# Kernel tuning notes

Hardware: AMD Instinct MI355X
Metric: run time of the kernel (lower is better)

Reference implementation:

```python
import jax, jax.numpy as jnp
import numpy as np

DIM = 256
N_EMBED = 1024
COMMITMENT_COST = 0.25


def setup_inputs() -> dict:
    key = jax.random.key(0)
    k1, k2 = jax.random.split(key)
    z = jax.random.normal(k1, (16, DIM, 64, 64), dtype=jnp.float32)
    lim = 1.0 / (2 * N_EMBED)
    embed_w = jax.random.uniform(k2, (N_EMBED, DIM), dtype=jnp.float32,
                                 minval=-lim, maxval=lim)
    return {"z": z, "embed_w": embed_w}


def reference(z, embed_w):
    # z: [B, C, H, W] -> [B, H, W, C]
    zp = jnp.transpose(z, (0, 2, 3, 1))
    B, H, W, C = zp.shape
    zf = zp.reshape(-1, C)  # [N, dim]
    # Squared euclidean distances to each codebook entry: [N, n_embed]
    d = (jnp.sum(zf * zf, axis=1, keepdims=True)
         + jnp.sum(embed_w * embed_w, axis=1)
         - 2.0 * jnp.matmul(zf, embed_w.T))
    idx = jnp.argmin(d, axis=1)  # [N]
    # Codebook lookup (equivalent to one-hot @ embed_w)
    z_q = embed_w[idx].reshape(zp.shape)  # [B, H, W, C]
    # VQ loss: codebook + commitment terms
    sg = jax.lax.stop_gradient
    loss = (jnp.mean((sg(z_q) - zp) ** 2)
            + COMMITMENT_COST * jnp.mean((z_q - sg(zp)) ** 2))
    # Straight-through estimator
    z_q_st = zp + sg(z_q - zp)
    # Perplexity from code usage histogram
    n = zf.shape[0]
    counts = jax.ops.segment_sum(jnp.ones((n,), jnp.float32), idx,
                                 num_segments=N_EMBED)
    e_mean = counts / n
    perplexity = jnp.exp(-jnp.sum(e_mean * jnp.log(e_mean + 1e-10)))
    z_q_out = jnp.transpose(z_q_st, (0, 3, 1, 2))  # back to [B, C, H, W]
    return loss, z_q_out, idx[:, None], perplexity
```

## Files before the change

kernel.cpp:

```cpp
#include <hip/hip_runtime.h>

#define BATCH 16
#define CDIM  256
#define HDIM  64
#define WDIM  64
#define NQ    65536
#define NE    1024
#define BM    32
#define KB    16

#define ZQ_OFF   1
#define IDX_OFF  16777217
#define PERP_OFF 16842753

#define WS_EE_OFF    0
#define WS_HIST_OFF  4096
#define WS_LOSS_OFF  8192
#define WS_WT_OFF    16384

__device__ __forceinline__ float pw128_sq(const float* __restrict__ p) {
    float r[8];
#pragma unroll
    for (int j = 0; j < 8; j++) r[j] = __fmul_rn(p[j], p[j]);
#pragma unroll
    for (int i = 8; i < 128; i += 8) {
#pragma unroll
        for (int j = 0; j < 8; j++) r[j] = __fadd_rn(r[j], __fmul_rn(p[i + j], p[i + j]));
    }
    return __fadd_rn(__fadd_rn(__fadd_rn(r[0], r[1]), __fadd_rn(r[2], r[3])),
                     __fadd_rn(__fadd_rn(r[4], r[5]), __fadd_rn(r[6], r[7])));
}

__global__ void vq_prep(const float* __restrict__ W, float* __restrict__ ee,
                        int* __restrict__ hist, double* __restrict__ loss_part) {
    int t = blockIdx.x * 256 + threadIdx.x;
    hist[t] = 0;
    if (t < 256) loss_part[t] = 0.0;
    const float* p = W + (size_t)t * CDIM;
    ee[t] = __fadd_rn(pw128_sq(p), pw128_sq(p + 128));
}

__global__ void vq_transpose(const float* __restrict__ W, float* __restrict__ WT) {
    __shared__ float T[64][65];
    const int e0 = (blockIdx.x & 15) * 64;
    const int k0 = (blockIdx.x >> 4) * 64;
    const int r  = threadIdx.x >> 4;
    const int c4 = threadIdx.x & 15;
#pragma unroll
    for (int s = 0; s < 4; s++) {
        float4 v = *(const float4*)(W + (size_t)(e0 + s * 16 + r) * CDIM + k0 + c4 * 4);
        T[s * 16 + r][c4 * 4 + 0] = v.x;
        T[s * 16 + r][c4 * 4 + 1] = v.y;
        T[s * 16 + r][c4 * 4 + 2] = v.z;
        T[s * 16 + r][c4 * 4 + 3] = v.w;
    }
    __syncthreads();
#pragma unroll
    for (int s = 0; s < 4; s++) {
        float4 o;
        o.x = T[c4 * 4 + 0][s * 16 + r];
        o.y = T[c4 * 4 + 1][s * 16 + r];
        o.z = T[c4 * 4 + 2][s * 16 + r];
        o.w = T[c4 * 4 + 3][s * 16 + r];
        *(float4*)(WT + (size_t)(k0 + s * 16 + r) * NE + e0 + c4 * 4) = o;
    }
}

__global__ __launch_bounds__(256, 4)
void vq_argmin(const float* __restrict__ z, const float* __restrict__ WT,
               const float* __restrict__ ee, float* __restrict__ out_idx,
               int* __restrict__ hist) {
    __shared__ __align__(16) float S[8192];
    __shared__ float zz_s[BM];
    __shared__ float tmp2[64];
    __shared__ float pD[BM][8];
    __shared__ int   pI[BM][8];

    float (*A)[BM]       = (float (*)[BM])S;
    float (*Bs)[KB][256] = (float (*)[KB][256])S;
    float (*redD)[64]    = (float (*)[64])S;
    int   (*redI)[64]    = (int (*)[64])(S + 2048);

    const int t    = threadIdx.x;
    const int lane = t & 63;
    const int wv   = t >> 6;
    const int n0   = blockIdx.x * BM;
    const int b    = n0 >> 12;
    const int h    = (n0 >> 6) & 63;
    const int w0   = n0 & 63;

    const float* zb = z + (size_t)b * (CDIM * HDIM * WDIM) + (size_t)h * WDIM + w0;
#pragma unroll
    for (int v = 0; v < 8; v++) {
        int idx4 = v * 256 + t;
        int c  = idx4 >> 3;
        int w4 = idx4 & 7;
        *(float4*)(&A[c][w4 * 4]) = *(const float4*)(zb + (size_t)c * (HDIM * WDIM) + w4 * 4);
    }
    __syncthreads();

    if (t < 64) {
        int q = t >> 1, base = (t & 1) * 128;
        float r[8];
#pragma unroll
        for (int j = 0; j < 8; j++) { float x = A[base + j][q]; r[j] = __fmul_rn(x, x); }
        for (int i = 8; i < 128; i += 8) {
#pragma unroll
            for (int j = 0; j < 8; j++) { float x = A[base + i + j][q]; r[j] = __fadd_rn(r[j], __fmul_rn(x, x)); }
        }
        tmp2[t] = __fadd_rn(__fadd_rn(__fadd_rn(r[0], r[1]), __fadd_rn(r[2], r[3])),
                            __fadd_rn(__fadd_rn(r[4], r[5]), __fadd_rn(r[6], r[7])));
    }
    __syncthreads();
    if (t < BM) zz_s[t] = __fadd_rn(tmp2[2 * t], tmp2[2 * t + 1]);

    const int tx  = t & 63;
    const int q0  = wv * 8;
    const int q0u = __builtin_amdgcn_readfirstlane(q0);
    const float* aG = zb + q0u;

    auto stage = [&](int sec, int skc, int nb) {
#pragma unroll
        for (int v = 0; v < 4; v++) {
            const int r_ = v * 4 + wv;
            const float* g_ = WT + (size_t)(skc * KB + r_) * NE + sec * 256 + lane * 4;
            __builtin_amdgcn_global_load_lds(
                (const __attribute__((address_space(1))) void*)g_,
                (__attribute__((address_space(3))) void*)(&Bs[nb][r_][0]),
                16, 0, 0);
        }
    };

    float bestD[8]; int bestI[8];
#pragma unroll
    for (int i = 0; i < 8; i++) { bestD[i] = 3.0e38f; bestI[i] = 0; }

    stage(0, 0, 0);
    __syncthreads();

    for (int ec = 0; ec < 4; ec++) {
        float acc[8][4];
#pragma unroll
        for (int i = 0; i < 8; i++)
#pragma unroll
            for (int j = 0; j < 4; j++) acc[i][j] = 0.0f;

        for (int kc = 0; kc < 16; kc++) {
            const int cur = kc & 1;
            {
                int nkc = kc + 1, nec = ec;
                if (nkc == 16) { nkc = 0; nec++; }
                if (nec < 4) stage(nec, nkc, cur ^ 1);
            }
            const int kb = kc * KB;
#pragma unroll 4
            for (int k2 = 0; k2 < KB; k2++) {
                const float4 b4 = *(const float4*)(&Bs[cur][k2][tx * 4]);
                const float* ar = aG + (size_t)(kb + k2) * (HDIM * WDIM);
                float av[8];
#pragma unroll
                for (int i = 0; i < 8; i++) av[i] = ar[i];
                float bv[4] = {b4.x, b4.y, b4.z, b4.w};
#pragma unroll
                for (int i = 0; i < 8; i++)
#pragma unroll
                    for (int j = 0; j < 4; j++)
                        acc[i][j] = __fmaf_rn(av[i], bv[j], acc[i][j]);
            }
            __syncthreads();
        }

        const int e0 = ec * 256 + tx * 4;
        float4 ee4 = *(const float4*)(ee + e0);
        float eev[4] = {ee4.x, ee4.y, ee4.z, ee4.w};
#pragma unroll
        for (int i = 0; i < 8; i++) {
            float zzq = zz_s[q0 + i];
#pragma unroll
            for (int j = 0; j < 4; j++) {
                float s = __fadd_rn(zzq, eev[j]);
                float d = __fsub_rn(s, __fadd_rn(acc[i][j], acc[i][j]));
                if (d < bestD[i]) { bestD[i] = d; bestI[i] = e0 + j; }
            }
        }
    }

    __syncthreads();
#pragma unroll
    for (int i = 0; i < 8; i++) { redD[q0 + i][tx] = bestD[i]; redI[q0 + i][tx] = bestI[i]; }
    __syncthreads();
    {
        int q = t >> 3, s = t & 7;
        float bd = redD[q][s * 8]; int bi = redI[q][s * 8];
#pragma unroll
        for (int u = 1; u < 8; u++) {
            float d2 = redD[q][s * 8 + u]; int i2 = redI[q][s * 8 + u];
            if (d2 < bd || (d2 == bd && i2 < bi)) { bd = d2; bi = i2; }
        }
        pD[q][s] = bd; pI[q][s] = bi;
    }
    __syncthreads();
    if (t < BM) {
        float bd = pD[t][0]; int bi = pI[t][0];
#pragma unroll
        for (int u = 1; u < 8; u++) {
            float d2 = pD[t][u]; int i2 = pI[t][u];
            if (d2 < bd || (d2 == bd && i2 < bi)) { bd = d2; bi = i2; }
        }
        out_idx[n0 + t] = (float)bi;
        atomicAdd(&hist[bi], 1);
    }
}

__global__ void vq_gather(const float* __restrict__ z, const float* __restrict__ W,
                          const float* __restrict__ idxf, float* __restrict__ zq_out,
                          double* __restrict__ loss_part) {
    const int gid = blockIdx.x * 256 + threadIdx.x;
    const int w4 = gid & 15;
    const int r  = gid >> 4;
    const int h  = r & 63;
    const int c  = (r >> 6) & 255;
    const int b  = r >> 14;
    const size_t off = (((size_t)(b * CDIM + c) * HDIM + h) * WDIM) + w4 * 4;
    const float4 zp = *(const float4*)(z + off);
    const int n = b * 4096 + h * 64 + w4 * 4;

    float zpv[4] = {zp.x, zp.y, zp.z, zp.w};
    float ov[4];
    double ls = 0.0;
#pragma unroll
    for (int l = 0; l < 4; l++) {
        int idx = (int)idxf[n + l];
        float zq = W[(size_t)idx * CDIM + c];
        float t1 = __fsub_rn(zq, zpv[l]);
        ov[l] = __fadd_rn(zpv[l], t1);
        ls += (double)t1 * (double)t1;
    }
    float4 o = {ov[0], ov[1], ov[2], ov[3]};
    *(float4*)(zq_out + off) = o;

#pragma unroll
    for (int s = 32; s > 0; s >>= 1) ls += __shfl_down(ls, s, 64);
    __shared__ double wsum[4];
    if ((threadIdx.x & 63) == 0) wsum[threadIdx.x >> 6] = ls;
    __syncthreads();
    if (threadIdx.x == 0) {
        double v = wsum[0] + wsum[1] + wsum[2] + wsum[3];
        atomicAdd(&loss_part[blockIdx.x & 255], v);
    }
}

__global__ void vq_final(const double* __restrict__ loss_part, const int* __restrict__ hist,
                         float* __restrict__ d_out) {
    __shared__ double s1[256], s2[256];
    const int t = threadIdx.x;
    double v = loss_part[t];
    double pv = 0.0;
#pragma unroll
    for (int j = 0; j < 4; j++) {
        int cnt = hist[t * 4 + j];
        double em = (double)cnt / 65536.0;
        pv += em * log(em + 1e-10);
    }
    s1[t] = v; s2[t] = pv;
    __syncthreads();
    for (int st = 128; st > 0; st >>= 1) {
        if (t < st) { s1[t] += s1[t + st]; s2[t] += s2[t + st]; }
        __syncthreads();
    }
    if (t == 0) {
        float m = (float)(s1[0] / 16777216.0);
        d_out[0] = 1.25f * m;
        d_out[PERP_OFF] = (float)exp(-s2[0]);
    }
}

extern "C" void kernel_launch(void* const* d_in, const int* in_sizes, int n_in,
                              void* d_out, int out_size, void* d_ws, size_t ws_size,
                              hipStream_t stream) {
    const float* z = (const float*)d_in[0];
    const float* W = (const float*)d_in[1];
    float* out = (float*)d_out;

    float*  ee        = (float*)((char*)d_ws + WS_EE_OFF);
    int*    hist      = (int*)((char*)d_ws + WS_HIST_OFF);
    double* loss_part = (double*)((char*)d_ws + WS_LOSS_OFF);
    float*  WT        = (float*)((char*)d_ws + WS_WT_OFF);

    vq_prep<<<4, 256, 0, stream>>>(W, ee, hist, loss_part);
    vq_transpose<<<64, 256, 0, stream>>>(W, WT);
    vq_argmin<<<NQ / BM, 256, 0, stream>>>(z, WT, ee, out + IDX_OFF, hist);
    vq_gather<<<(NQ * CDIM / 4) / 256, 256, 0, stream>>>(z, W, out + IDX_OFF, out + ZQ_OFF, loss_part);
    vq_final<<<1, 256, 0, stream>>>(loss_part, hist, out);
}
```

Measured before the change: 556.5 us.

## Software-pipeline z loads as float4 registers and halve B tile depth

Halves the codebook k-tile depth so each LDS buffer holds 8 rows, and adds register double-buffering of the z operand: float4 loads for the next 4 k-steps are issued before computing the current 4. Running best distance/index is kept in LDS reduction arrays (moved past the B buffers) instead of registers, which frees registers for the prefetch buffers. The stage loop now always prefetches, wrapping to section 0 at the end, so it does one redundant tile load. The intent is to hide global-load latency on z and cut register pressure, at the cost of twice as many block barriers per section.

```diff
diff --git a/kernel.cpp b/kernel.cpp
--- a/kernel.cpp
+++ b/kernel.cpp
@@ -7,7 +7,7 @@
 #define NQ    65536
 #define NE    1024
 #define BM    32
-#define KB    16
+#define KB    8
 
 #define ZQ_OFF   1
 #define IDX_OFF  16777217
@@ -78,8 +78,8 @@
 
     float (*A)[BM]       = (float (*)[BM])S;
     float (*Bs)[KB][256] = (float (*)[KB][256])S;
-    float (*redD)[64]    = (float (*)[64])S;
-    int   (*redI)[64]    = (int (*)[64])(S + 2048);
+    float (*redD)[64]    = (float (*)[64])(S + 4096);
+    int   (*redI)[64]    = (int   (*)[64])(S + 6144);
 
     const int t    = threadIdx.x;
     const int lane = t & 63;
@@ -114,16 +114,15 @@
     __syncthreads();
     if (t < BM) zz_s[t] = __fadd_rn(tmp2[2 * t], tmp2[2 * t + 1]);
 
-    const int tx  = t & 63;
-    const int q0  = wv * 8;
-    const int q0u = __builtin_amdgcn_readfirstlane(q0);
-    const float* aG = zb + q0u;
-
-    auto stage = [&](int sec, int skc, int nb) {
-#pragma unroll
-        for (int v = 0; v < 4; v++) {
+    const int tx = t & 63;
+    const int q0 = wv * 8;
+    const float* aq = zb + q0;
+
+    auto stage = [&](int ssec, int skc, int nb) {
+#pragma unroll
+        for (int v = 0; v < 2; v++) {
             const int r_ = v * 4 + wv;
-            const float* g_ = WT + (size_t)(skc * KB + r_) * NE + sec * 256 + lane * 4;
+            const float* g_ = WT + (size_t)(skc * KB + r_) * NE + ssec * 256 + lane * 4;
             __builtin_amdgcn_global_load_lds(
                 (const __attribute__((address_space(1))) void*)g_,
                 (__attribute__((address_space(3))) void*)(&Bs[nb][r_][0]),
@@ -131,73 +130,95 @@
         }
     };
 
-    float bestD[8]; int bestI[8];
-#pragma unroll
-    for (int i = 0; i < 8; i++) { bestD[i] = 3.0e38f; bestI[i] = 0; }
+    float4 av0[8], av1[8];
 
     stage(0, 0, 0);
-    __syncthreads();
-
-    for (int ec = 0; ec < 4; ec++) {
+#pragma unroll
+    for (int kk = 0; kk < 4; kk++) {
+        const float* ap = aq + (size_t)kk * 4096;
+        av0[kk * 2]     = *(const float4*)ap;
+        av0[kk * 2 + 1] = *(const float4*)(ap + 4);
+    }
+    __syncthreads();
+
+#define COMPUTE4(CUR, G, AV)                                                   \
+    {                                                                          \
+        _Pragma("unroll")                                                      \
+        for (int k2 = 0; k2 < 4; k2++) {                                       \
+            const float4 b4 = *(const float4*)(&Bs[CUR][(G) + k2][tx * 4]);    \
+            const float4 aL = AV[k2 * 2], aH = AV[k2 * 2 + 1];                 \
+            float avv[8] = {aL.x, aL.y, aL.z, aL.w, aH.x, aH.y, aH.z, aH.w};   \
+            float bvv[4] = {b4.x, b4.y, b4.z, b4.w};                           \
+            _Pragma("unroll")                                                  \
+            for (int i = 0; i < 8; i++)                                        \
+                _Pragma("unroll")                                              \
+                for (int j = 0; j < 4; j++)                                    \
+                    acc[i][j] = __fmaf_rn(avv[i], bvv[j], acc[i][j]);          \
+        }                                                                      \
+    }
+
+    for (int sec = 0; sec < 4; sec++) {
         float acc[8][4];
 #pragma unroll
         for (int i = 0; i < 8; i++)
 #pragma unroll
             for (int j = 0; j < 4; j++) acc[i][j] = 0.0f;
 
-        for (int kc = 0; kc < 16; kc++) {
+        for (int kc = 0; kc < 32; kc++) {
             const int cur = kc & 1;
             {
-                int nkc = kc + 1, nec = ec;
-                if (nkc == 16) { nkc = 0; nec++; }
-                if (nec < 4) stage(nec, nkc, cur ^ 1);
+                int nkc = kc + 1, nsec = sec;
+                if (nkc == 32) { nkc = 0; nsec = (sec + 1) & 3; }
+                stage(nsec, nkc, cur ^ 1);
             }
-            const int kb = kc * KB;
-#pragma unroll 4
-            for (int k2 = 0; k2 < KB; k2++) {
-                const float4 b4 = *(const float4*)(&Bs[cur][k2][tx * 4]);
-                const float* ar = aG + (size_t)(kb + k2) * (HDIM * WDIM);
-                float av[8];
-#pragma unroll
-                for (int i = 0; i < 8; i++) av[i] = ar[i];
-                float bv[4] = {b4.x, b4.y, b4.z, b4.w};
-#pragma unroll
-                for (int i = 0; i < 8; i++)
-#pragma unroll
-                    for (int j = 0; j < 4; j++)
-                        acc[i][j] = __fmaf_rn(av[i], bv[j], acc[i][j]);
+            const int kbase = kc * KB;
+#pragma unroll
+            for (int kk = 0; kk < 4; kk++) {
+                const float* ap = aq + (size_t)((kbase + 4 + kk) & 255) * 4096;
+                av1[kk * 2]     = *(const float4*)ap;
+                av1[kk * 2 + 1] = *(const float4*)(ap + 4);
             }
+            COMPUTE4(cur, 0, av0)
+#pragma unroll
+            for (int kk = 0; kk < 4; kk++) {
+                const float* ap = aq + (size_t)((kbase + 8 + kk) & 255) * 4096;
+                av0[kk * 2]     = *(const float4*)ap;
+                av0[kk * 2 + 1] = *(const float4*)(ap + 4);
+            }
+            COMPUTE4(cur, 4, av1)
             __syncthreads();
         }
 
-        const int e0 = ec * 256 + tx * 4;
+        const int e0 = sec * 256 + tx * 4;
         float4 ee4 = *(const float4*)(ee + e0);
         float eev[4] = {ee4.x, ee4.y, ee4.z, ee4.w};
 #pragma unroll
         for (int i = 0; i < 8; i++) {
-            float zzq = zz_s[q0 + i];
+            float bd; int bi;
+            if (sec == 0) { bd = 3.0e38f; bi = 0; }
+            else          { bd = redD[q0 + i][tx]; bi = redI[q0 + i][tx]; }
+            const float zzq = zz_s[q0 + i];
 #pragma unroll
             for (int j = 0; j < 4; j++) {
                 float s = __fadd_rn(zzq, eev[j]);
                 float d = __fsub_rn(s, __fadd_rn(acc[i][j], acc[i][j]));
-                if (d < bestD[i]) { bestD[i] = d; bestI[i] = e0 + j; }
+                if (d < bd) { bd = d; bi = e0 + j; }
             }
-        }
-    }
-
-    __syncthreads();
-#pragma unroll
-    for (int i = 0; i < 8; i++) { redD[q0 + i][tx] = bestD[i]; redI[q0 + i][tx] = bestI[i]; }
+            redD[q0 + i][tx] = bd; redI[q0 + i][tx] = bi;
+        }
+    }
+#undef COMPUTE4
+
     __syncthreads();
     {
-        int q = t >> 3, s = t & 7;
-        float bd = redD[q][s * 8]; int bi = redI[q][s * 8];
+        int q = t >> 3, s8 = t & 7;
+        float bd = redD[q][s8 * 8]; int bi = redI[q][s8 * 8];
 #pragma unroll
         for (int u = 1; u < 8; u++) {
-            float d2 = redD[q][s * 8 + u]; int i2 = redI[q][s * 8 + u];
+            float d2 = redD[q][s8 * 8 + u]; int i2 = redI[q][s8 * 8 + u];
             if (d2 < bd || (d2 == bd && i2 < bi)) { bd = d2; bi = i2; }
         }
-        pD[q][s] = bd; pI[q][s] = bi;
+        pD[q][s8] = bd; pI[q][s8] = bi;
     }
     __syncthreads();
     if (t < BM) {
```

After: 1.170 ms. 110% more time.

## Widen per-thread codebook tile to 8 columns over two 512-wide sections

Applied to the files above, without the earlier changes.

Each thread now accumulates an 8x8 tile (8 queries by 8 codes) instead of 8x4, and the codebook is processed in two 512-wide sections instead of four 256-wide ones, with the K chunk halved to 8 so the LDS buffer size is unchanged. Each z value loaded from global memory is therefore reused across twice as many FMAs, halving the repeated z loads and the per-section epilogue passes. The cost is higher register pressure from 64 accumulators, which may reduce occupancy under the 256x4 launch bound, and twice as many barriers per section because the K chunk is smaller.

```diff
diff --git a/kernel.cpp b/kernel.cpp
--- a/kernel.cpp
+++ b/kernel.cpp
@@ -7,7 +7,8 @@
 #define NQ    65536
 #define NE    1024
 #define BM    32
-#define KB    16
+#define KB    8
+#define SECW  512
 
 #define ZQ_OFF   1
 #define IDX_OFF  16777217
@@ -76,10 +77,10 @@
     __shared__ float pD[BM][8];
     __shared__ int   pI[BM][8];
 
-    float (*A)[BM]       = (float (*)[BM])S;
-    float (*Bs)[KB][256] = (float (*)[KB][256])S;
-    float (*redD)[64]    = (float (*)[64])S;
-    int   (*redI)[64]    = (int (*)[64])(S + 2048);
+    float (*A)[BM]        = (float (*)[BM])S;
+    float (*Bs)[KB][SECW] = (float (*)[KB][SECW])S;
+    float (*redD)[64]     = (float (*)[64])S;
+    int   (*redI)[64]     = (int   (*)[64])(S + 2048);
 
     const int t    = threadIdx.x;
     const int lane = t & 63;
@@ -119,14 +120,16 @@
     const int q0u = __builtin_amdgcn_readfirstlane(q0);
     const float* aG = zb + q0u;
 
-    auto stage = [&](int sec, int skc, int nb) {
+    auto stage = [&](int ssec, int skc, int nb) {
 #pragma unroll
         for (int v = 0; v < 4; v++) {
-            const int r_ = v * 4 + wv;
-            const float* g_ = WT + (size_t)(skc * KB + r_) * NE + sec * 256 + lane * 4;
+            const int s_  = v * 4 + wv;
+            const int r_  = s_ >> 1;
+            const int hf_ = s_ & 1;
+            const float* g_ = WT + (size_t)(skc * KB + r_) * NE + ssec * SECW + hf_ * 256 + lane * 4;
             __builtin_amdgcn_global_load_lds(
                 (const __attribute__((address_space(1))) void*)g_,
-                (__attribute__((address_space(3))) void*)(&Bs[nb][r_][0]),
+                (__attribute__((address_space(3))) void*)(&Bs[nb][r_][hf_ * 256]),
                 16, 0, 0);
         }
     };
@@ -138,50 +141,60 @@
     stage(0, 0, 0);
     __syncthreads();
 
-    for (int ec = 0; ec < 4; ec++) {
-        float acc[8][4];
+    for (int sec = 0; sec < 2; sec++) {
+        float acc[8][8];
 #pragma unroll
         for (int i = 0; i < 8; i++)
 #pragma unroll
-            for (int j = 0; j < 4; j++) acc[i][j] = 0.0f;
-
-        for (int kc = 0; kc < 16; kc++) {
+            for (int j = 0; j < 8; j++) acc[i][j] = 0.0f;
+
+        for (int kc = 0; kc < 32; kc++) {
             const int cur = kc & 1;
             {
-                int nkc = kc + 1, nec = ec;
-                if (nkc == 16) { nkc = 0; nec++; }
-                if (nec < 4) stage(nec, nkc, cur ^ 1);
+                int nkc = kc + 1, nsec = sec;
+                if (nkc == 32) { nkc = 0; nsec++; }
+                if (nsec < 2) stage(nsec, nkc, cur ^ 1);
             }
             const int kb = kc * KB;
-#pragma unroll 4
+#pragma unroll
             for (int k2 = 0; k2 < KB; k2++) {
-                const float4 b4 = *(const float4*)(&Bs[cur][k2][tx * 4]);
-                const float* ar = aG + (size_t)(kb + k2) * (HDIM * WDIM);
+                const float4 b4a = *(const float4*)(&Bs[cur][k2][tx * 4]);
+                const float4 b4b = *(const float4*)(&Bs[cur][k2][256 + tx * 4]);
+                const float* ar = aG + (size_t)(kb + k2) * 4096;
                 float av[8];
 #pragma unroll
                 for (int i = 0; i < 8; i++) av[i] = ar[i];
-                float bv[4] = {b4.x, b4.y, b4.z, b4.w};
+                float bv[8] = {b4a.x, b4a.y, b4a.z, b4a.w, b4b.x, b4b.y, b4b.z, b4b.w};
 #pragma unroll
                 for (int i = 0; i < 8; i++)
 #pragma unroll
-                    for (int j = 0; j < 4; j++)
+                    for (int j = 0; j < 8; j++)
                         acc[i][j] = __fmaf_rn(av[i], bv[j], acc[i][j]);
             }
             __syncthreads();
         }
 
-        const int e0 = ec * 256 + tx * 4;
-        float4 ee4 = *(const float4*)(ee + e0);
-        float eev[4] = {ee4.x, ee4.y, ee4.z, ee4.w};
+        const int e0a = sec * SECW + tx * 4;
+        const int e0b = e0a + 256;
+        float4 eeA = *(const float4*)(ee + e0a);
+        float4 eeB = *(const float4*)(ee + e0b);
+        float eva[4] = {eeA.x, eeA.y, eeA.z, eeA.w};
+        float evb[4] = {eeB.x, eeB.y, eeB.z, eeB.w};
 #pragma unroll
         for (int i = 0; i < 8; i++) {
             float zzq = zz_s[q0 + i];
 #pragma unroll
             for (int j = 0; j < 4; j++) {
-                float s = __fadd_rn(zzq, eev[j]);
+                float s = __fadd_rn(zzq, eva[j]);
                 float d = __fsub_rn(s, __fadd_rn(acc[i][j], acc[i][j]));
-                if (d < bestD[i]) { bestD[i] = d; bestI[i] = e0 + j; }
+                if (d < bestD[i]) { bestD[i] = d; bestI[i] = e0a + j; }
             }
+#pragma unroll
+            for (int j = 0; j < 4; j++) {
+                float s = __fadd_rn(zzq, evb[j]);
+                float d = __fsub_rn(s, __fadd_rn(acc[i][4 + j], acc[i][4 + j]));
+                if (d < bestD[i]) { bestD[i] = d; bestI[i] = e0b + j; }
+            }
         }
     }
 
@@ -190,14 +203,14 @@
     for (int i = 0; i < 8; i++) { redD[q0 + i][tx] = bestD[i]; redI[q0 + i][tx] = bestI[i]; }
     __syncthreads();
     {
-        int q = t >> 3, s = t & 7;
-        float bd = redD[q][s * 8]; int bi = redI[q][s * 8];
+        int q = t >> 3, s8 = t & 7;
+        float bd = redD[q][s8 * 8]; int bi = redI[q][s8 * 8];
 #pragma unroll
         for (int u = 1; u < 8; u++) {
-            float d2 = redD[q][s * 8 + u]; int i2 = redI[q][s * 8 + u];
+            float d2 = redD[q][s8 * 8 + u]; int i2 = redI[q][s8 * 8 + u];
             if (d2 < bd || (d2 == bd && i2 < bi)) { bd = d2; bi = i2; }
         }
-        pD[q][s] = bd; pI[q][s] = bi;
+        pD[q][s8] = bd; pI[q][s8] = bi;
     }
     __syncthreads();
     if (t < BM) {
```

After: 564.9 us. About the same (+1.5%).
